# Performance work log

Hardware: AMD Instinct MI355X
Metric: run time of the kernel (lower is better)

Reference implementation:

```python
import jax, jax.numpy as jnp
import numpy as np
from jax import lax

# Static config (matches init_kwargs / electrode montage)
B, T, V = 16, 1536, 64
F1, D, H = 16, 2, 4
F2 = F1 * D              # 32
FO = F2 // H             # 8, GAT per-head out dim
K1, K3 = 32, 16          # conv kernel sizes (temporal)
P1, P2 = 8, 4            # avg pool sizes
KNN = 4
EPS = 1e-5
NEG_SLOPE = 0.2          # PyG GATConv leaky_relu slope


def _build_edges():
    # deterministic electrode geometry -> kNN graph, plus PyG self-loops
    rng = np.random.RandomState(0)
    pos = rng.randn(V, 3)
    dmat = np.linalg.norm(pos[:, None] - pos[None, :], axis=-1)
    order = np.argsort(dmat, axis=1)
    nbrs = order[:, 1:KNN + 1]                      # exclude self
    src = np.repeat(np.arange(V), KNN)
    dst = nbrs.reshape(-1)
    # add self loops (GATConv default add_self_loops=True)
    src = np.concatenate([src, np.arange(V)])
    dst = np.concatenate([dst, np.arange(V)])
    return jnp.asarray(np.stack([src, dst]), dtype=jnp.int32)  # (2, E)


def _bn(x, g, b, m, v, axis):
    shp = [1] * x.ndim
    shp[axis] = -1
    rs = lambda a: a.reshape(shp)
    return rs(g) * (x - rs(m)) * lax.rsqrt(rs(v) + EPS) + rs(b)


def _conv_same_t(x, w, k):
    # Conv2d(..., (1,k), padding='same'): torch pads (k-1)//2 left, rest right
    lp = (k - 1) // 2
    return lax.conv_general_dilated(x, w, (1, 1), [(0, 0), (lp, k - 1 - lp)],
                                    dimension_numbers=('NCHW', 'OIHW', 'NCHW'))


def _gat(x, W, a_src, a_dst, bias, src, dst):
    # Batched PyG GATConv (eval mode, dropout off), concat heads.
    # x: (Ng, V, F1); W: (F1, H*FO); a_src/a_dst: (H, FO); bias: (H*FO,)
    Ng = x.shape[0]
    h = jnp.einsum('nvf,fho->nvho', x, W.reshape(F1, H, FO))   # (Ng,V,H,FO)
    es = jnp.einsum('nvho,ho->nvh', h, a_src)[:, src]          # (Ng,E,H)
    ed = jnp.einsum('nvho,ho->nvh', h, a_dst)[:, dst]
    e = jax.nn.leaky_relu(es + ed, NEG_SLOPE)
    # softmax over incoming edges of each target node (segment softmax)
    m = jnp.full((Ng, V, H), -1e30, e.dtype).at[:, dst].max(e)
    ex = jnp.exp(e - m[:, dst])
    den = jnp.zeros((Ng, V, H), e.dtype).at[:, dst].add(ex)
    alpha = ex / den[:, dst]                                   # (Ng,E,H)
    out = jnp.zeros((Ng, V, H, FO), e.dtype).at[:, dst].add(alpha[..., None] * h[:, src])
    return out.reshape(Ng, V, H * FO) + bias


def setup_inputs() -> dict:
    key = jax.random.key(0)
    ks = jax.random.split(key, 16)
    bn = lambda k, c: (1.0 + 0.1 * jax.random.normal(jax.random.fold_in(k, 0), (c,)),
                       0.1 * jax.random.normal(jax.random.fold_in(k, 1), (c,)),
                       0.1 * jax.random.normal(jax.random.fold_in(k, 2), (c,)),
                       0.5 + jax.random.uniform(jax.random.fold_in(k, 3), (c,)))
    bn1 = bn(ks[1], F1); bn2 = bn(ks[2], F2); bn3 = bn(ks[3], F2)
    inp = {
        'x': jax.random.normal(ks[0], (B, 1, V, T), jnp.float32),
        'conv1_w': 0.1 * jax.random.normal(ks[4], (F1, 1, 1, K1), jnp.float32),
        'bn1_g': bn1[0], 'bn1_b': bn1[1], 'bn1_m': bn1[2], 'bn1_v': bn1[3],
        'gat_w': (1.0 / np.sqrt(F1)) * jax.random.normal(ks[5], (F1, H * FO), jnp.float32),
        'gat_asrc': 0.3 * jax.random.normal(ks[6], (H, FO), jnp.float32),
        'gat_adst': 0.3 * jax.random.normal(ks[7], (H, FO), jnp.float32),
        'gat_bias': 0.05 * jax.random.normal(ks[8], (H * FO,), jnp.float32),
        'bn2_g': bn2[0], 'bn2_b': bn2[1], 'bn2_m': bn2[2], 'bn2_v': bn2[3],
        'conv3_w': 0.1 * jax.random.normal(ks[9], (F2, F2, 1, K3), jnp.float32),
        'bn3_g': bn3[0], 'bn3_b': bn3[1], 'bn3_m': bn3[2], 'bn3_v': bn3[3],
        'edge_index': _build_edges(),
    }
    return inp


def reference(x, conv1_w, bn1_g, bn1_b, bn1_m, bn1_v,
              gat_w, gat_asrc, gat_adst, gat_bias,
              bn2_g, bn2_b, bn2_m, bn2_v,
              conv3_w, bn3_g, bn3_b, bn3_m, bn3_v, edge_index):
    src, dst = edge_index[0], edge_index[1]
    # block1: temporal conv + BN
    h = _conv_same_t(x, conv1_w, K1)                 # (B,F1,V,T)
    h = _bn(h, bn1_g, bn1_b, bn1_m, bn1_v, 1)
    # spatial GNN over B*T independent electrode graphs
    xg = h.transpose(0, 3, 2, 1).reshape(B * T, V, F1)
    g = _gat(xg, gat_w, gat_asrc, gat_adst, gat_bias, src, dst)   # (BT,V,F2)
    g = g.mean(axis=1).reshape(B, T, F2).transpose(0, 2, 1)       # (B,F2,T)
    g = _bn(g, bn2_g, bn2_b, bn2_m, bn2_v, 1)[:, :, None, :]      # (B,F2,1,T)
    # tail: elu -> pool -> conv -> bn -> elu -> pool (dropout = eval no-op)
    h = jax.nn.elu(g)
    h = h.reshape(B, F2, 1, T // P1, P1).mean(-1)
    h = _conv_same_t(h, conv3_w, K3)
    h = _bn(h, bn3_g, bn3_b, bn3_m, bn3_v, 1)
    h = jax.nn.elu(h)
    h = h.reshape(B, F2, 1, T // P1 // P2, P2).mean(-1)           # (B,F2,1,48)
    return h
```

## Files before the change

### kernel.cpp

```cpp
#include <hip/hip_runtime.h>
#include <math.h>

#define TPB 256

constexpr int Bc = 16, Tc = 1536;
constexpr int T2c = 192;
constexpr float EPSc = 1e-5f;
constexpr float NSLOPE = 0.2f;
constexpr int MDI = 16;
constexpr int MDO = 8;

constexpr int OW_WEFF = 0;
constexpr int OW_CHL  = 1024;
constexpr int OW_CES  = 1056;
constexpr int OW_WES  = 1064;
constexpr int OW_WED  = 1192;
constexpr int OW_A2C2 = 1320;
constexpr int OW_GRAPH= 1384;
constexpr int OW_P    = 1801;

constexpr int GB_INTS = 417;

constexpr int L_XT  = 0;
constexpr int L_WB  = 2720;
constexpr int L_Y   = 4896;
constexpr int L_GR  = 6208;
constexpr int L_TOT = 6625;

__global__ void prep_kernel(const float* __restrict__ c1w,
                            const float* __restrict__ g1, const float* __restrict__ b1,
                            const float* __restrict__ m1, const float* __restrict__ v1,
                            const float* __restrict__ W,
                            const float* __restrict__ asrc, const float* __restrict__ adst,
                            const float* __restrict__ bias,
                            const float* __restrict__ g2, const float* __restrict__ b2,
                            const float* __restrict__ m2, const float* __restrict__ v2,
                            const int* __restrict__ ei, int ne, float* __restrict__ ws)
{
    const int tid = threadIdx.x;
    __shared__ float sweff[1024];
    __shared__ float schl[32];
    __shared__ int isrcp_i[64 * MDI];
    __shared__ int outdst_i[64 * MDO];
    __shared__ int inslot[64], outslot[64];

    for (int idx = tid; idx < 1024; idx += TPB) {
        int k = idx >> 5, f2 = idx & 31;
        float s = 0.f;
        for (int f = 0; f < 16; f++) {
            float a1 = g1[f] * rsqrtf(v1[f] + EPSc);
            s += a1 * W[f * 32 + f2] * c1w[f * 32 + k];
        }
        ws[OW_WEFF + idx] = s;
        sweff[idx] = s;
    }
    for (int f2 = tid; f2 < 32; f2 += TPB) {
        float s = 0.f;
        for (int f = 0; f < 16; f++) {
            float a1 = g1[f] * rsqrtf(v1[f] + EPSc);
            s = fmaf(b1[f] - a1 * m1[f], W[f * 32 + f2], s);
        }
        ws[OW_CHL + f2] = s;
        schl[f2] = s;
        float a2 = g2[f2] * rsqrtf(v2[f2] + EPSc);
        ws[OW_A2C2 + f2] = a2;
        ws[OW_A2C2 + 32 + f2] = b2[f2] + a2 * (bias[f2] - m2[f2]);
    }

    for (int i = tid; i < 64 * MDI; i += TPB) isrcp_i[i] = 0;
    for (int i = tid; i < 64 * MDO; i += TPB) outdst_i[i] = 0;
    if (tid < 64) { inslot[tid] = 0; outslot[tid] = 0; }
    __syncthreads();
    for (int e = tid; e < ne; e += TPB) {
        int s = ei[e], d = ei[ne + e];
        int pi = atomicAdd(&inslot[d], 1);
        if (pi < MDI) isrcp_i[d * MDI + pi] = s;
        int po = atomicAdd(&outslot[s], 1);
        if (po < MDO) outdst_i[s * MDO + po] = d;
    }
    __syncthreads();

    if (tid < 128) {
        int k = tid >> 2, h = tid & 3;
        float s1 = 0.f, s2 = 0.f;
        for (int o = 0; o < 8; o++) {
            float wv = sweff[k * 32 + h * 8 + o];
            s1 = fmaf(asrc[h * 8 + o], wv, s1);
            s2 = fmaf(adst[h * 8 + o], wv, s2);
        }
        ws[OW_WES + h * 32 + k] = s1;
        ws[OW_WED + h * 32 + k] = s2;
    }
    if (tid < 4) {
        float s1 = 0.f, s2 = 0.f;
        for (int o = 0; o < 8; o++) {
            float cv = schl[tid * 8 + o];
            s1 = fmaf(asrc[tid * 8 + o], cv, s1);
            s2 = fmaf(adst[tid * 8 + o], cv, s2);
        }
        ws[OW_CES + tid] = s1;
        ws[OW_CES + 4 + tid] = s2;
    }
    unsigned char* gb = (unsigned char*)(ws + OW_GRAPH);
    for (int i = tid; i < 64 * MDI; i += TPB) gb[i] = (unsigned char)isrcp_i[i];
    for (int i = tid; i < 64 * MDO; i += TPB) gb[1088 + i] = (unsigned char)outdst_i[i];
    if (tid < 64) {
        gb[1024 + tid] = (unsigned char)(inslot[tid] < MDI ? inslot[tid] : MDI);
        gb[1600 + tid] = (unsigned char)(outslot[tid] < MDO ? outslot[tid] : MDO);
    }
    __syncthreads();
    if (tid == 0) {
        int mi = 0, mo = 0;
        for (int d = 0; d < 64; d++) {
            int a = gb[1024 + d], o = gb[1600 + d];
            mi = a > mi ? a : mi;
            mo = o > mo ? o : mo;
        }
        gb[1664] = (unsigned char)mi;
        gb[1665] = (unsigned char)mo;
    }
}

__global__ __launch_bounds__(TPB, 4) void gat_kernel(
    const float* __restrict__ x,
    const float* __restrict__ wfp,
    const float* __restrict__ chlp,
    const float* __restrict__ cesg,
    const float* __restrict__ wesg,
    const float* __restrict__ wedg,
    const float* __restrict__ a2c2,
    const int* __restrict__ graphi,
    float* __restrict__ pout)
{
    __shared__ __align__(16) float sm[L_TOT];
    unsigned char* gb = (unsigned char*)&sm[L_GR];

    const int tid  = threadIdx.x;
    const int b    = blockIdx.x / 192;
    const int tile = blockIdx.x % 192;
    const int t0   = tile * 8;

    const int h = tid >> 6, v = tid & 63;

    for (int idx = tid; idx < GB_INTS; idx += TPB) ((int*)&sm[L_GR])[idx] = graphi[idx];
    for (int idx = tid; idx < 2560; idx += TPB) {
        const int vv = idx / 40, j = idx % 40;
        float val = 1.0f;
        if (j < 39) {
            const int t = t0 - 15 + j;
            val = (t >= 0 && t < Tc) ? x[(b * 64 + vv) * Tc + t] : 0.f;
        }
        sm[L_XT + j * 68 + vv] = val;
    }
    __syncthreads();

    const int hs = __builtin_amdgcn_readfirstlane(h);
    const float* wesh = wesg + hs * 32;
    const float* wedh = wedg + hs * 32;

    float aes[8], aed[8];
    {
        const float cesh = cesg[hs], cedh = cesg[4 + hs];
        #pragma unroll
        for (int t = 0; t < 8; t++) { aes[t] = cesh; aed[t] = cedh; }
        float xr[8];
        #pragma unroll
        for (int q = 0; q < 7; q++) xr[q] = sm[L_XT + q * 68 + v];
        #pragma unroll
        for (int k = 0; k < 32; k++) {
            xr[(k + 7) & 7] = sm[L_XT + (k + 7) * 68 + v];
            const float wek = wesh[k];
            const float wdk = wedh[k];
            #pragma unroll
            for (int t = 0; t < 8; t++) {
                const float xv = xr[(k + t) & 7];
                aes[t] = fmaf(xv, wek, aes[t]);
                aed[t] = fmaf(xv, wdk, aed[t]);
            }
        }
    }

    {
        const int indeg = gb[1024 + v];
        const int mdin  = gb[1664];
        float den[8] = { 0.f,0.f,0.f,0.f,0.f,0.f,0.f,0.f };
        for (int e = 0; e < mdin; e++) {
            const int s = gb[v * MDI + e];
            const float valid = (e < indeg) ? 1.f : 0.f;
            #pragma unroll
            for (int t = 0; t < 8; t++) {
                float ev = __shfl(aes[t], s) + aed[t];
                ev = ev > 0.f ? ev : NSLOPE * ev;
                den[t] += valid * __expf(ev);
            }
        }
        float rden[8];
        #pragma unroll
        for (int t = 0; t < 8; t++) rden[t] = 1.f / den[t];

        const int odeg = gb[1600 + v];
        const int mdo  = gb[1665];
        float wb[8] = { 0.f,0.f,0.f,0.f,0.f,0.f,0.f,0.f };
        for (int j = 0; j < mdo; j++) {
            const int d = gb[1088 + v * MDO + j];
            const float valid = (j < odeg) ? 1.f : 0.f;
            #pragma unroll
            for (int t = 0; t < 8; t++) {
                float ev = aes[t] + __shfl(aed[t], d);
                ev = ev > 0.f ? ev : NSLOPE * ev;
                wb[t] += valid * __expf(ev) * __shfl(rden[t], d);
            }
        }
        #pragma unroll
        for (int t = 0; t < 8; t++) sm[L_WB + h * 544 + t * 68 + v] = wb[t];
    }
    __asm__ volatile("s_waitcnt lgkmcnt(0)" ::: "memory");

    {
        const int vh = v >> 5, tp = (v >> 3) & 3, cg = v & 7;
        float ya[2][5] = { { 0.f,0.f,0.f,0.f,0.f }, { 0.f,0.f,0.f,0.f,0.f } };
        const float* xbase = &sm[L_XT + cg * 5 * 68 + vh * 32];
        const float* wb0   = &sm[L_WB + h * 544 + (2 * tp) * 68 + vh * 32];
        #pragma unroll
        for (int v4 = 0; v4 < 8; v4++) {
            const float4 wa = *(const float4*)(wb0 + v4 * 4);
            const float4 wbv = *(const float4*)(wb0 + 68 + v4 * 4);
            #pragma unroll
            for (int q = 0; q < 5; q++) {
                const float4 x4 = *(const float4*)(xbase + q * 68 + v4 * 4);
                ya[0][q] = fmaf(wa.x, x4.x, fmaf(wa.y, x4.y,
                           fmaf(wa.z, x4.z, fmaf(wa.w, x4.w, ya[0][q]))));
                ya[1][q] = fmaf(wbv.x, x4.x, fmaf(wbv.y, x4.y,
                           fmaf(wbv.z, x4.z, fmaf(wbv.w, x4.w, ya[1][q]))));
            }
        }
        #pragma unroll
        for (int i = 0; i < 2; i++)
            #pragma unroll
            for (int q = 0; q < 5; q++)
                ya[i][q] += __shfl_xor(ya[i][q], 32);
        if (vh == 0) {
            float* yr = &sm[L_Y + h * 328 + (2 * tp) * 41 + cg * 5];
            #pragma unroll
            for (int i = 0; i < 2; i++)
                #pragma unroll
                for (int q = 0; q < 5; q++)
                    yr[i * 41 + q] = ya[i][q];
        }
    }
    __asm__ volatile("s_waitcnt lgkmcnt(0)" ::: "memory");

    {
        const int t = v >> 3, o = v & 7;
        const int f2d = h * 8 + o;
        float wfr[32];
        #pragma unroll
        for (int k = 0; k < 32; k++) wfr[k] = wfp[k * 32 + f2d];

        const float* yr = &sm[L_Y + h * 328 + t * 41];
        float acc = chlp[f2d] * yr[39];
        #pragma unroll
        for (int k = 0; k < 32; k++)
            acc = fmaf(wfr[k], yr[t + k], acc);

        const float a2 = a2c2[f2d], c2 = a2c2[32 + f2d];
        float y = fmaf(a2, acc * (1.f / 64.f), c2);
        y = y > 0.f ? y : __expf(y) - 1.f;
        y += __shfl_xor(y, 8);
        y += __shfl_xor(y, 16);
        y += __shfl_xor(y, 32);
        if (v < 8)
            pout[(b * T2c + tile) * 32 + h * 8 + v] = y * 0.125f;
    }
}

__global__ __launch_bounds__(TPB) void conv3_kernel(const float* __restrict__ pp,
                                                    const float* __restrict__ w3,
                                                    const float* __restrict__ g3,
                                                    const float* __restrict__ b3,
                                                    const float* __restrict__ m3,
                                                    const float* __restrict__ v3,
                                                    float* __restrict__ outp)
{
    __shared__ float pl[63 * 32];
    __shared__ float q[48 * 32];
    const int tid = threadIdx.x;
    const int b = blockIdx.x >> 2, cc = blockIdx.x & 3;

    for (int idx = tid; idx < 63 * 32; idx += TPB) {
        int r = idx >> 5, f2 = idx & 31;
        int tog = cc * 48 - 7 + r;
        pl[idx] = (tog >= 0 && tog < T2c) ? pp[(b * T2c + tog) * 32 + f2] : 0.f;
    }
    __syncthreads();

    const int f2o = tid & 31, grp = tid >> 5;
    const int tb = grp * 6;
    float acc[6] = { 0.f, 0.f, 0.f, 0.f, 0.f, 0.f };
    for (int f2i = 0; f2i < 32; f2i++) {
        float seg[21];
        #pragma unroll
        for (int r = 0; r < 21; r++) seg[r] = pl[(tb + r) * 32 + f2i];
        const float4* wrow = (const float4*)(w3 + (f2o * 32 + f2i) * 16);
        #pragma unroll
        for (int k4 = 0; k4 < 4; k4++) {
            const float4 w4 = wrow[k4];
            #pragma unroll
            for (int j = 0; j < 6; j++) {
                acc[j] = fmaf(seg[j + k4 * 4 + 0], w4.x,
                         fmaf(seg[j + k4 * 4 + 1], w4.y,
                         fmaf(seg[j + k4 * 4 + 2], w4.z,
                         fmaf(seg[j + k4 * 4 + 3], w4.w, acc[j]))));
            }
        }
    }
    const float a3 = g3[f2o] * rsqrtf(v3[f2o] + EPSc);
    const float c3 = b3[f2o] - a3 * m3[f2o];
    #pragma unroll
    for (int j = 0; j < 6; j++) {
        float y = fmaf(a3, acc[j], c3);
        y = y > 0.f ? y : __expf(y) - 1.f;
        q[(tb + j) * 32 + f2o] = y;
    }
    __syncthreads();
    for (int idx = tid; idx < 12 * 32; idx += TPB) {
        int t4 = idx >> 5, f2 = idx & 31;
        int r0 = t4 * 4;
        float s = q[r0 * 32 + f2] + q[(r0 + 1) * 32 + f2] +
                  q[(r0 + 2) * 32 + f2] + q[(r0 + 3) * 32 + f2];
        outp[(b * 32 + f2) * 48 + cc * 12 + t4] = s * 0.25f;
    }
}

extern "C" void kernel_launch(void* const* d_in, const int* in_sizes, int n_in,
                              void* d_out, int out_size, void* d_ws, size_t ws_size,
                              hipStream_t stream)
{
    const float* x    = (const float*)d_in[0];
    const float* c1w  = (const float*)d_in[1];
    const float* g1   = (const float*)d_in[2];
    const float* b1   = (const float*)d_in[3];
    const float* m1   = (const float*)d_in[4];
    const float* v1   = (const float*)d_in[5];
    const float* W    = (const float*)d_in[6];
    const float* asrc = (const float*)d_in[7];
    const float* adst = (const float*)d_in[8];
    const float* bias = (const float*)d_in[9];
    const float* g2   = (const float*)d_in[10];
    const float* b2   = (const float*)d_in[11];
    const float* m2   = (const float*)d_in[12];
    const float* v2   = (const float*)d_in[13];
    const float* w3   = (const float*)d_in[14];
    const float* g3   = (const float*)d_in[15];
    const float* b3   = (const float*)d_in[16];
    const float* m3   = (const float*)d_in[17];
    const float* v3   = (const float*)d_in[18];
    const int*   ei   = (const int*)d_in[19];
    const int    ne   = in_sizes[19] / 2;

    float* ws = (float*)d_ws;

    prep_kernel<<<1, TPB, 0, stream>>>(c1w, g1, b1, m1, v1, W, asrc, adst,
                                       bias, g2, b2, m2, v2, ei, ne, ws);

    gat_kernel<<<Bc * T2c, TPB, 0, stream>>>(x,
                                             ws + OW_WEFF, ws + OW_CHL,
                                             ws + OW_CES,
                                             ws + OW_WES, ws + OW_WED,
                                             ws + OW_A2C2,
                                             (const int*)(ws + OW_GRAPH),
                                             ws + OW_P);

    conv3_kernel<<<Bc * 4, TPB, 0, stream>>>(ws + OW_P, w3, g3, b3, m3, v3,
                                             (float*)d_out);
}
```

Measured before the change: 166.5 us.

## Compute GAT softmax denominators via LDS atomics over out-edges, reusing exponentials

Replaces the separate in-edge loop that computed softmax denominators with a scatter of out-edge exponentials into per-head LDS buffers using atomicAdd. The exponentials are computed once and reused for both the denominator and the weighted sum. Logits are prescaled by log2(e) so that exp2 can be used, and the reciprocal uses rcp plus one Newton step. It relies on a fixed out-degree bound of 5 and on wave-local synchronisation through lgkmcnt waits; LDS atomics and per-step waits could serialise.

```diff
diff --git a/kernel.cpp b/kernel.cpp
--- a/kernel.cpp
+++ b/kernel.cpp
@@ -9,6 +9,8 @@
 constexpr float NSLOPE = 0.2f;
 constexpr int MDI = 16;
 constexpr int MDO = 8;
+constexpr int NOUT = 5;
+constexpr float L2E = 1.4426950408889634f;
 
 constexpr int OW_WEFF = 0;
 constexpr int OW_CHL  = 1024;
@@ -178,41 +180,43 @@
                 aed[t] = fmaf(xv, wdk, aed[t]);
             }
         }
+        #pragma unroll
+        for (int t = 0; t < 8; t++) { aes[t] *= L2E; aed[t] *= L2E; }
     }
 
     {
-        const int indeg = gb[1024 + v];
-        const int mdin  = gb[1664];
-        float den[8] = { 0.f,0.f,0.f,0.f,0.f,0.f,0.f,0.f };
-        for (int e = 0; e < mdin; e++) {
-            const int s = gb[v * MDI + e];
-            const float valid = (e < indeg) ? 1.f : 0.f;
-            #pragma unroll
-            for (int t = 0; t < 8; t++) {
-                float ev = __shfl(aes[t], s) + aed[t];
-                ev = ev > 0.f ? ev : NSLOPE * ev;
-                den[t] += valid * __expf(ev);
+        float* denb = &sm[L_GR + (h << 6)];
+        const int odeg = gb[1600 + v];
+        int   dj[NOUT];
+        float va[NOUT];
+        #pragma unroll
+        for (int j = 0; j < NOUT; j++) {
+            dj[j] = gb[1088 + v * MDO + j];
+            va[j] = (j < odeg) ? 1.f : 0.f;
+        }
+
+        denb[v] = 0.f;
+        #pragma unroll
+        for (int t = 0; t < 8; t++) {
+            float E[NOUT];
+            #pragma unroll
+            for (int j = 0; j < NOUT; j++) {
+                float ev = aes[t] + __shfl(aed[t], dj[j]);
+                ev = fmaxf(ev, NSLOPE * ev);
+                E[j] = va[j] * __builtin_amdgcn_exp2f(ev);
             }
-        }
-        float rden[8];
-        #pragma unroll
-        for (int t = 0; t < 8; t++) rden[t] = 1.f / den[t];
-
-        const int odeg = gb[1600 + v];
-        const int mdo  = gb[1665];
-        float wb[8] = { 0.f,0.f,0.f,0.f,0.f,0.f,0.f,0.f };
-        for (int j = 0; j < mdo; j++) {
-            const int d = gb[1088 + v * MDO + j];
-            const float valid = (j < odeg) ? 1.f : 0.f;
-            #pragma unroll
-            for (int t = 0; t < 8; t++) {
-                float ev = aes[t] + __shfl(aed[t], d);
-                ev = ev > 0.f ? ev : NSLOPE * ev;
-                wb[t] += valid * __expf(ev) * __shfl(rden[t], d);
-            }
-        }
-        #pragma unroll
-        for (int t = 0; t < 8; t++) sm[L_WB + h * 544 + t * 68 + v] = wb[t];
+            #pragma unroll
+            for (int j = 0; j < NOUT; j++) atomicAdd(&denb[dj[j]], E[j]);
+            __asm__ volatile("s_waitcnt lgkmcnt(0)" ::: "memory");
+            const float den = denb[v];
+            denb[v] = 0.f;
+            float r = __builtin_amdgcn_rcpf(den);
+            r = r * (2.f - den * r);
+            float wbv = 0.f;
+            #pragma unroll
+            for (int j = 0; j < NOUT; j++) wbv = fmaf(E[j], __shfl(r, dj[j]), wbv);
+            sm[L_WB + h * 544 + t * 68 + v] = wbv;
+        }
     }
     __asm__ volatile("s_waitcnt lgkmcnt(0)" ::: "memory");
 
```

After: 308.6 us. +85.3%, slower.
